# Kernel tuning notes

Measured on AMD Instinct MI355X. Metric: run time of the kernel, lower is better.

Reference implementation:

```python
import jax, jax.numpy as jnp
import numpy as np

B, S, D, H = 2, 2048, 1024, 16
DK = D // H
ROPE_BASE = 10000.0


def setup_inputs() -> dict:
    key = jax.random.key(0)
    ks = jax.random.split(key, 6)
    x = jax.random.normal(ks[0], (B, S, D), dtype=jnp.float32)
    # causal mask, broadcastable to [B,H,S,S]; masked_fill where mask==0
    mask = jnp.tril(jnp.ones((S, S), dtype=bool))[None, None]
    position_ids = jnp.tile(jnp.arange(S, dtype=jnp.int32)[None, :], (B, 1))
    sc = 1.0 / np.sqrt(D)
    Wq = jax.random.normal(ks[1], (D, D), dtype=jnp.float32) * sc
    Wk = jax.random.normal(ks[2], (D, D), dtype=jnp.float32) * sc
    Wv = jax.random.normal(ks[3], (D, D), dtype=jnp.float32) * sc
    Wo = jax.random.normal(ks[4], (D, D), dtype=jnp.float32) * sc
    bo = jnp.zeros((D,), dtype=jnp.float32)
    return {"x": x, "mask": mask, "position_ids": position_ids,
            "Wq": Wq, "Wk": Wk, "Wv": Wv, "Wo": Wo, "bo": bo}


def _rotate_half(t):
    t1, t2 = t[..., : t.shape[-1] // 2], t[..., t.shape[-1] // 2:]
    return jnp.concatenate((-t2, t1), axis=-1)


def reference(x, mask, position_ids, Wq, Wk, Wv, Wo, bo):
    b, s, d = x.shape
    h, dk = H, DK
    scale = 1.0 / np.sqrt(dk)

    def proj(W):  # torch Linear: x @ W.T -> [b,h,s,dk]
        return (x @ W.T).reshape(b, s, h, dk).transpose(0, 2, 1, 3)

    Q, K, V = proj(Wq), proj(Wk), proj(Wv)

    # rotary tables (computed in fp32, matching RotaryEmbedding)
    inv_freq = 1.0 / (ROPE_BASE ** (jnp.arange(0, dk, 2, dtype=jnp.float32) / dk))
    t = jnp.arange(s, dtype=jnp.float32)
    freqs = jnp.outer(t, inv_freq)            # [s, dk/2]
    emb = jnp.concatenate((freqs, freqs), -1) # [s, dk]
    cos = jnp.cos(emb)[position_ids][:, None]  # [b,1,s,dk]
    sin = jnp.sin(emb)[position_ids][:, None]
    Q = Q * cos + _rotate_half(Q) * sin
    K = K * cos + _rotate_half(K) * sin

    scores = jnp.einsum('bhqd,bhkd->bhqk', Q, K) * scale
    scores = jnp.where(mask, scores, jnp.float32(-1e9))
    attn = jax.nn.softmax(scores, axis=-1)  # dropout is identity in eval
    out = jnp.einsum('bhqk,bhkd->bhqd', attn, V)
    out = out.transpose(0, 2, 1, 3).reshape(b, s, d)
    return out @ Wo.T + bo
```

## Files before the change

kernel.cpp:

```cpp
#include <hip/hip_runtime.h>
#include <hip/hip_bf16.h>
#include <cstdint>

#define BB 2
#define SS 2048
#define DD 1024
#define HH 16
#define DK 64
#define MROWS (BB*SS)
#define NQKV  (3*DD)

typedef __bf16 bf16x8 __attribute__((ext_vector_type(8)));
typedef float  f32x4  __attribute__((ext_vector_type(4)));
typedef float  f32x16 __attribute__((ext_vector_type(16)));
typedef unsigned u32x2 __attribute__((ext_vector_type(2)));

static __device__ __forceinline__ unsigned short f2bf(float f) {
    __bf16 h = (__bf16)f;
    return __builtin_bit_cast(unsigned short, h);
}
static __device__ __forceinline__ float bf2f(unsigned short u) {
    return (float)__builtin_bit_cast(__bf16, u);
}

#define GLOAD16(gsrc, ldst) \
    __builtin_amdgcn_global_load_lds((const __attribute__((address_space(1))) void*)(gsrc), \
                                     (__attribute__((address_space(3))) void*)(ldst), 16, 0, 0)

static __device__ __forceinline__ void pl32_swap(unsigned &x, unsigned &y) {
#if __has_builtin(__builtin_amdgcn_permlane32_swap)
    u32x2 r = __builtin_amdgcn_permlane32_swap(x, y, false, false);
    x = r[0]; y = r[1];
#else
    asm volatile("v_permlane32_swap_b32 %0, %1" : "+v"(x), "+v"(y));
#endif
}
static __device__ __forceinline__ float swap_half(float v, bool hi) {
    unsigned x = __builtin_bit_cast(unsigned, v), y = x;
    pl32_swap(x, y);
    return __builtin_bit_cast(float, hi ? x : y);
}
template<int BASE> static __device__ __forceinline__ bf16x8 cvt_chunk(const f32x16 &p) {
    unsigned x0, y0, x1, y1;
    asm("v_cvt_pk_bf16_f32 %0, %1, %2" : "=v"(x0) : "v"(p[BASE+0]), "v"(p[BASE+1]));
    asm("v_cvt_pk_bf16_f32 %0, %1, %2" : "=v"(y0) : "v"(p[BASE+4]), "v"(p[BASE+5]));
    asm("v_cvt_pk_bf16_f32 %0, %1, %2" : "=v"(x1) : "v"(p[BASE+2]), "v"(p[BASE+3]));
    asm("v_cvt_pk_bf16_f32 %0, %1, %2" : "=v"(y1) : "v"(p[BASE+6]), "v"(p[BASE+7]));
    pl32_swap(x0, y0);
    pl32_swap(x1, y1);
    union { unsigned u[4]; bf16x8 v; } r;
    r.u[0] = x0; r.u[1] = x1; r.u[2] = y0; r.u[3] = y1;
    return r.v;
}

__global__ void cast_all(const float* __restrict__ x,  const float* __restrict__ wq,
                         const float* __restrict__ wk, const float* __restrict__ wv,
                         const float* __restrict__ wo,
                         unsigned short* __restrict__ xb, unsigned short* __restrict__ wqkv,
                         unsigned short* __restrict__ wob)
{
    const int NX = MROWS * DD;
    const int NW = DD * DD;
    const int total = (NX + 4 * NW) / 8;
    for (int i = blockIdx.x * blockDim.x + threadIdx.x; i < total; i += gridDim.x * blockDim.x) {
        int base = i * 8;
        const float* src; unsigned short* dst; int off;
        if      (base < NX)          { src = x;  dst = xb;          off = base; }
        else if (base < NX + NW)     { src = wq; dst = wqkv;        off = base - NX; }
        else if (base < NX + 2*NW)   { src = wk; dst = wqkv + NW;   off = base - NX - NW; }
        else if (base < NX + 3*NW)   { src = wv; dst = wqkv + 2*NW; off = base - NX - 2*NW; }
        else                         { src = wo; dst = wob;         off = base - NX - 3*NW; }
        float4 a = *(const float4*)(src + off);
        float4 b = *(const float4*)(src + off + 4);
        union { unsigned short s[8]; uint4 v; } u;
        u.s[0] = f2bf(a.x); u.s[1] = f2bf(a.y); u.s[2] = f2bf(a.z); u.s[3] = f2bf(a.w);
        u.s[4] = f2bf(b.x); u.s[5] = f2bf(b.y); u.s[6] = f2bf(b.z); u.s[7] = f2bf(b.w);
        *(uint4*)(dst + off) = u.v;
    }
}

__global__ void rope_table(float* __restrict__ tabc, float* __restrict__ tabs)
{
    int i = blockIdx.x * blockDim.x + threadIdx.x;
    int s = i >> 5, d = i & 31;
    float inv = exp2f(-(float)d * (13.287712379549449f / 32.f));
    float ang = (float)s * inv;
    tabc[i] = cosf(ang);
    tabs[i] = sinf(ang);
}

template<int OUTF32>
__global__ __launch_bounds__(256) void gemm_bt(
    const unsigned short* __restrict__ A, const unsigned short* __restrict__ Bm,
    void* __restrict__ Cout, const float* __restrict__ bias,
    int M, int N, int K)
{
    __shared__ __align__(16) unsigned short sA[128 * 64];
    __shared__ __align__(16) unsigned short sB[128 * 64];
    const int tid = threadIdx.x;
    const int w = tid >> 6, l = tid & 63;
    const int wm = w >> 1, wn = w & 1;
    const int lr = l & 15, lg = l >> 4;
    const int mBase = blockIdx.y * 128, nBase = blockIdx.x * 128;
    const int srow = tid >> 3;
    const int skof = (tid & 7) * 8;

    f32x4 acc[4][4] = {};

    for (int kt = 0; kt < K; kt += 64) {
        __syncthreads();
        #pragma unroll
        for (int i = 0; i < 4; ++i) {
            const unsigned short* srcA = A + (size_t)(mBase + i*32 + srow) * K + kt + skof;
            GLOAD16(srcA, &sA[i*2048 + w*512]);
            const unsigned short* srcB = Bm + (size_t)(nBase + i*32 + srow) * K + kt + skof;
            GLOAD16(srcB, &sB[i*2048 + w*512]);
        }
        __syncthreads();
        #pragma unroll
        for (int kk = 0; kk < 2; ++kk) {
            bf16x8 af[4], bfv[4];
            #pragma unroll
            for (int mi = 0; mi < 4; ++mi)
                af[mi] = *(const bf16x8*)&sA[(wm*64 + mi*16 + lr)*64 + kk*32 + lg*8];
            #pragma unroll
            for (int ni = 0; ni < 4; ++ni)
                bfv[ni] = *(const bf16x8*)&sB[(wn*64 + ni*16 + lr)*64 + kk*32 + lg*8];
            #pragma unroll
            for (int mi = 0; mi < 4; ++mi)
                #pragma unroll
                for (int ni = 0; ni < 4; ++ni)
                    acc[mi][ni] = __builtin_amdgcn_mfma_f32_16x16x32_bf16(af[mi], bfv[ni], acc[mi][ni], 0, 0, 0);
        }
    }
    #pragma unroll
    for (int mi = 0; mi < 4; ++mi) {
        #pragma unroll
        for (int j = 0; j < 4; ++j) {
            int row = mBase + wm*64 + mi*16 + lg*4 + j;
            #pragma unroll
            for (int ni = 0; ni < 4; ++ni) {
                int col = nBase + wn*64 + ni*16 + lr;
                float v = acc[mi][ni][j];
                if (OUTF32) ((float*)Cout)[(size_t)row * N + col] = v + bias[col];
                else        ((unsigned short*)Cout)[(size_t)row * N + col] = f2bf(v);
            }
        }
    }
}

__global__ void rope_qk(const unsigned short* __restrict__ qkv,
                        const int* __restrict__ pids,
                        const float* __restrict__ tabc, const float* __restrict__ tabs,
                        unsigned short* __restrict__ Qb, unsigned short* __restrict__ Kb)
{
    int i = blockIdx.x * blockDim.x + threadIdx.x;
    int cb = i & 3;
    int h  = (i >> 2) & 15;
    int isK = (i >> 6) & 1;
    int r  = i >> 7;
    int pos = pids[r];
    int dbase = cb * 8;

    const unsigned short* src = qkv + (size_t)r * NQKV + isK * DD + h * 64 + dbase;
    union { unsigned short u[8]; uint4 v; } a, bq, o1, o2;
    a.v  = *(const uint4*)src;
    bq.v = *(const uint4*)(src + 32);
    float cs[8], sn[8];
    *(float4*)&cs[0] = *(const float4*)(tabc + pos*32 + dbase);
    *(float4*)&cs[4] = *(const float4*)(tabc + pos*32 + dbase + 4);
    *(float4*)&sn[0] = *(const float4*)(tabs + pos*32 + dbase);
    *(float4*)&sn[4] = *(const float4*)(tabs + pos*32 + dbase + 4);
    float scale = isK ? 1.0f : 0.1803368801111244f;
    #pragma unroll
    for (int j = 0; j < 8; ++j) {
        float v1 = bf2f(a.u[j]), v2 = bf2f(bq.u[j]);
        o1.u[j] = f2bf((v1*cs[j] - v2*sn[j]) * scale);
        o2.u[j] = f2bf((v2*cs[j] + v1*sn[j]) * scale);
    }
    unsigned short* dst = (isK ? Kb : Qb) + (size_t)r * DD + h * 64 + dbase;
    *(uint4*)dst        = o1.v;
    *(uint4*)(dst + 32) = o2.v;
}

__global__ __launch_bounds__(256) void v_transpose(
    const unsigned short* __restrict__ qkv, unsigned short* __restrict__ Vt)
{
    __shared__ __align__(16) unsigned short sT[64 * 64];
    const int bh = blockIdx.y;
    const int st = blockIdx.x;
    const int b = bh >> 4, h = bh & 15;
    const int tid = threadIdx.x;
    #pragma unroll
    for (int i = 0; i < 2; ++i) {
        int c = tid + i*256;
        int s = c >> 3, cb = c & 7;
        const unsigned short* src = qkv + (size_t)(b*SS + st*64 + s) * NQKV + 2*DD + h*64 + cb*8;
        uint4 v = *(const uint4*)src;
        *(uint4*)&sT[s*64 + ((cb ^ (s >> 3)) * 8)] = v;
    }
    __syncthreads();
    #pragma unroll
    for (int i = 0; i < 2; ++i) {
        int c = tid + i*256;
        int d = c >> 3, sb = c & 7;
        union { unsigned short u[8]; uint4 v; } o;
        #pragma unroll
        for (int e = 0; e < 8; ++e) {
            int s = sb*8 + e;
            o.u[e] = sT[s*64 + (((d >> 3) ^ (s >> 3)) * 8) + (d & 7)];
        }
        *(uint4*)(Vt + (size_t)(bh*64 + d) * SS + st*64 + sb*8) = o.v;
    }
}

__global__ __launch_bounds__(128, 2) void attn_fwd(
    const unsigned short* __restrict__ Qb,
    const unsigned short* __restrict__ Kb,
    const unsigned short* __restrict__ Vt,
    unsigned short* __restrict__ Ob)
{
    __shared__ __align__(16) unsigned short sK[2][64 * 64];
    __shared__ __align__(16) unsigned short sV[2][64 * 64];
    const int tid = threadIdx.x;
    const int w = tid >> 6, l = tid & 63;
    const int lq = l & 31;
    const int hi5 = l >> 5;
    const bool hb = hi5 != 0;

    const int xcd = blockIdx.x & 7;
    const int c   = blockIdx.x >> 3;
    const int g   = c >> 5;
    const int s_  = c & 31;
    const int qt  = (g & 1) ? (31 - s_) : s_;
    const int bh  = xcd * 4 + g;
    const int b = bh >> 4, h = bh & 15;

    const int srow2 = tid >> 3;
    const int skof  = (tid & 7) * 8;
    const int sksw  = skof ^ ((srow2 & 7) * 8);
    const int sw    = (lq & 7) * 8;
    const float THR = 12.0f;

    const unsigned kR = (unsigned)((b*SS + srow2) * DD + h*64 + sksw);
    const unsigned vR = (unsigned)((bh*64 + srow2) * SS + sksw);

    bf16x8 qf[4];
    {
        const unsigned short* qp = Qb + (size_t)(b*SS + qt*64 + w*32 + lq) * DD + h*64 + hi5*8;
        #pragma unroll
        for (int dkc = 0; dkc < 4; ++dkc)
            qf[dkc] = *(const bf16x8*)(qp + dkc*16);
    }
    const int q_lane = qt*64 + w*32 + lq;

    f32x16 o0 = {}, o1 = {};
    float mrow = -3.0e38f, lsum = 0.f;
    int cur = 0;

    #pragma unroll
    for (int i = 0; i < 4; ++i) {
        GLOAD16(Kb + kR + (unsigned)(i << 14), &sK[0][i*1024 + w*512]);
        GLOAD16(Vt + vR + (unsigned)(i << 15), &sV[0][i*1024 + w*512]);
    }

    for (int kt = 0; kt <= qt; ++kt) {
        __syncthreads();
        if (kt < qt) {
            unsigned ko = (unsigned)(kt + 1) << 16;
            unsigned vo = (unsigned)(kt + 1) << 6;
            #pragma unroll
            for (int i = 0; i < 4; ++i) {
                GLOAD16(Kb + kR + ko + (unsigned)(i << 14), &sK[cur^1][i*1024 + w*512]);
                GLOAD16(Vt + vR + vo + (unsigned)(i << 15), &sV[cur^1][i*1024 + w*512]);
            }
        }

        f32x16 p0 = {}, p1 = {};
        __builtin_amdgcn_s_setprio(1);
        #pragma unroll
        for (int dkc = 0; dkc < 4; ++dkc) {
            bf16x8 k0 = *(const bf16x8*)&sK[cur][lq*64 + ((dkc*16 + hi5*8) ^ sw)];
            p0 = __builtin_amdgcn_mfma_f32_32x32x16_bf16(k0, qf[dkc], p0, 0, 0, 0);
        }
        #pragma unroll
        for (int dkc = 0; dkc < 4; ++dkc) {
            bf16x8 k1 = *(const bf16x8*)&sK[cur][(32 + lq)*64 + ((dkc*16 + hi5*8) ^ sw)];
            p1 = __builtin_amdgcn_mfma_f32_32x32x16_bf16(k1, qf[dkc], p1, 0, 0, 0);
        }
        __builtin_amdgcn_s_setprio(0);

        if (kt == qt) {
            const int kb0 = kt*64 + 4*hi5;
            #pragma unroll
            for (int r = 0; r < 16; ++r) {
                const int cr = (r & 3) + 8*(r >> 2);
                if (kb0 + cr > q_lane)      p0[r] = -1e30f;
                if (kb0 + 32 + cr > q_lane) p1[r] = -1e30f;
            }
        }

        float tt[16];
        #pragma unroll
        for (int r = 0; r < 16; ++r) tt[r] = fmaxf(p0[r], p1[r]);
        #pragma unroll
        for (int s2 = 8; s2 >= 1; s2 >>= 1)
            #pragma unroll
            for (int r = 0; r < 8; ++r)
                if (r < s2) tt[r] = fmaxf(tt[r], tt[r + s2]);
        float tmx = fmaxf(tt[0], swap_half(tt[0], hb));

        float growth = tmx - mrow;
        if (!__all(growth <= THR)) {
            float mnew = fmaxf(mrow, tmx);
            float alpha = exp2f(mrow - mnew);
            lsum *= alpha;
            mrow = mnew;
            #pragma unroll
            for (int r = 0; r < 16; ++r) { o0[r] *= alpha; o1[r] *= alpha; }
        }

        #pragma unroll
        for (int r = 0; r < 16; ++r) {
            p0[r] = exp2f(p0[r] - mrow);
            p1[r] = exp2f(p1[r] - mrow);
        }
        float st[16];
        #pragma unroll
        for (int r = 0; r < 16; ++r) st[r] = p0[r] + p1[r];
        #pragma unroll
        for (int s2 = 8; s2 >= 1; s2 >>= 1)
            #pragma unroll
            for (int r = 0; r < 8; ++r)
                if (r < s2) st[r] += st[r + s2];
        lsum += st[0];

        __builtin_amdgcn_s_setprio(1);
        {
            bf16x8 pa, vf;
            pa = cvt_chunk<0>(p0);
            vf = *(const bf16x8*)&sV[cur][lq*64 + ((0*16 + hi5*8) ^ sw)];
            o0 = __builtin_amdgcn_mfma_f32_32x32x16_bf16(vf, pa, o0, 0, 0, 0);
            vf = *(const bf16x8*)&sV[cur][(32 + lq)*64 + ((0*16 + hi5*8) ^ sw)];
            o1 = __builtin_amdgcn_mfma_f32_32x32x16_bf16(vf, pa, o1, 0, 0, 0);
            pa = cvt_chunk<8>(p0);
            vf = *(const bf16x8*)&sV[cur][lq*64 + ((1*16 + hi5*8) ^ sw)];
            o0 = __builtin_amdgcn_mfma_f32_32x32x16_bf16(vf, pa, o0, 0, 0, 0);
            vf = *(const bf16x8*)&sV[cur][(32 + lq)*64 + ((1*16 + hi5*8) ^ sw)];
            o1 = __builtin_amdgcn_mfma_f32_32x32x16_bf16(vf, pa, o1, 0, 0, 0);
            pa = cvt_chunk<0>(p1);
            vf = *(const bf16x8*)&sV[cur][lq*64 + ((2*16 + hi5*8) ^ sw)];
            o0 = __builtin_amdgcn_mfma_f32_32x32x16_bf16(vf, pa, o0, 0, 0, 0);
            vf = *(const bf16x8*)&sV[cur][(32 + lq)*64 + ((2*16 + hi5*8) ^ sw)];
            o1 = __builtin_amdgcn_mfma_f32_32x32x16_bf16(vf, pa, o1, 0, 0, 0);
            pa = cvt_chunk<8>(p1);
            vf = *(const bf16x8*)&sV[cur][lq*64 + ((3*16 + hi5*8) ^ sw)];
            o0 = __builtin_amdgcn_mfma_f32_32x32x16_bf16(vf, pa, o0, 0, 0, 0);
            vf = *(const bf16x8*)&sV[cur][(32 + lq)*64 + ((3*16 + hi5*8) ^ sw)];
            o1 = __builtin_amdgcn_mfma_f32_32x32x16_bf16(vf, pa, o1, 0, 0, 0);
        }
        __builtin_amdgcn_s_setprio(0);
        cur ^= 1;
    }

    __syncthreads();
    float ls = lsum + swap_half(lsum, hb);
    float inv = 1.f / ls;
    unsigned short* sO = &sK[0][0] + w * 2048;

    #pragma unroll
    for (int g2 = 0; g2 < 4; ++g2) {
        unsigned ua, ub; uint2 t2;
        float v0 = o0[g2*4+0]*inv, v1 = o0[g2*4+1]*inv, v2 = o0[g2*4+2]*inv, v3 = o0[g2*4+3]*inv;
        asm("v_cvt_pk_bf16_f32 %0, %1, %2" : "=v"(ua) : "v"(v0), "v"(v1));
        asm("v_cvt_pk_bf16_f32 %0, %1, %2" : "=v"(ub) : "v"(v2), "v"(v3));
        t2.x = ua; t2.y = ub;
        *(uint2*)&sO[lq*64 + g2*8 + hi5*4] = t2;
        float w0 = o1[g2*4+0]*inv, w1 = o1[g2*4+1]*inv, w2 = o1[g2*4+2]*inv, w3 = o1[g2*4+3]*inv;
        asm("v_cvt_pk_bf16_f32 %0, %1, %2" : "=v"(ua) : "v"(w0), "v"(w1));
        asm("v_cvt_pk_bf16_f32 %0, %1, %2" : "=v"(ub) : "v"(w2), "v"(w3));
        t2.x = ua; t2.y = ub;
        *(uint2*)&sO[lq*64 + 32 + g2*8 + hi5*4] = t2;
    }
    asm volatile("s_waitcnt lgkmcnt(0)" ::: "memory");
    __builtin_amdgcn_sched_barrier(0);

    const int row = l >> 1, cb2 = (l & 1) * 32;
    const unsigned short* sOr = sO + row*64 + cb2;
    unsigned short* gp = Ob + (size_t)(b*SS + qt*64 + w*32 + row) * DD + h*64 + cb2;
    #pragma unroll
    for (int c2 = 0; c2 < 4; ++c2)
        *(uint4*)(gp + c2*8) = *(const uint4*)(sOr + c2*8);
}

extern "C" void kernel_launch(void* const* d_in, const int* in_sizes, int n_in,
                              void* d_out, int out_size, void* d_ws, size_t ws_size,
                              hipStream_t stream)
{
    const float* x  = (const float*)d_in[0];
    const int* pids = (const int*)d_in[2];
    const float* wq = (const float*)d_in[3];
    const float* wk = (const float*)d_in[4];
    const float* wv = (const float*)d_in[5];
    const float* wo = (const float*)d_in[6];
    const float* bo = (const float*)d_in[7];
    float* out = (float*)d_out;

    char* ws = (char*)d_ws;
    unsigned short* xb   = (unsigned short*)(ws);
    unsigned short* wqkv = (unsigned short*)(ws + (size_t)( 8u<<20));
    unsigned short* wob  = (unsigned short*)(ws + (size_t)(14u<<20));
    unsigned short* qkvp = (unsigned short*)(ws + (size_t)(16u<<20));
    unsigned short* Qb   = (unsigned short*)(ws + (size_t)(40u<<20));
    unsigned short* Kb   = (unsigned short*)(ws + (size_t)(48u<<20));
    unsigned short* Vt   = (unsigned short*)(ws + (size_t)(56u<<20));
    float* tabc          = (float*)(ws + (size_t)(64u<<20));
    float* tabs          = (float*)(ws + (size_t)(64u<<20) + (256u<<10));
    unsigned short* Ob   = xb;

    cast_all<<<dim3(4096), dim3(256), 0, stream>>>(x, wq, wk, wv, wo, xb, wqkv, wob);
    rope_table<<<dim3(256), dim3(256), 0, stream>>>(tabc, tabs);
    gemm_bt<0><<<dim3(NQKV/128, MROWS/128), dim3(256), 0, stream>>>(
        xb, wqkv, (void*)qkvp, (const float*)nullptr, MROWS, NQKV, DD);
    rope_qk<<<dim3(2048), dim3(256), 0, stream>>>(qkvp, pids, tabc, tabs, Qb, Kb);
    v_transpose<<<dim3(32, 32), dim3(256), 0, stream>>>(qkvp, Vt);
    attn_fwd<<<dim3(1024), dim3(128), 0, stream>>>(Qb, Kb, Vt, Ob);
    gemm_bt<1><<<dim3(DD/128, MROWS/128), dim3(256), 0, stream>>>(
        Ob, wob, (void*)out, bo, MROWS, DD, DD);
}
```

Measured before the change: 154.2 us.

## Fuse RoPE into QKV GEMM epilogue and swizzle GEMM block order

The RoPE rotation and Q scaling move into the QKV projection GEMM epilogue, using the fact that each 64-column wave tile holds one head so the d and d+32 pairs sit in the same thread's accumulators. This removes the separate rope_qk kernel and the round trip of Q and K through the intermediate qkv buffer. V is now written to its own buffer. Both GEMMs also switch to a 1D grid with an XCD-aware swizzle of block indices, meant to improve L2 locality across the chiplets. The epilogue stores are scalar 2-byte writes, so the fused kernel may write less efficiently than the old vectorized rope kernel.

```diff
diff --git a/kernel.cpp b/kernel.cpp
--- a/kernel.cpp
+++ b/kernel.cpp
@@ -89,11 +89,12 @@
     tabs[i] = sinf(ang);
 }
 
-template<int OUTF32>
-__global__ __launch_bounds__(256) void gemm_bt(
+__global__ __launch_bounds__(256) void gemm_qkv(
     const unsigned short* __restrict__ A, const unsigned short* __restrict__ Bm,
-    void* __restrict__ Cout, const float* __restrict__ bias,
-    int M, int N, int K)
+    const int* __restrict__ pids,
+    const float* __restrict__ tabc, const float* __restrict__ tabs,
+    unsigned short* __restrict__ Qb, unsigned short* __restrict__ Kb,
+    unsigned short* __restrict__ Vr)
 {
     __shared__ __align__(16) unsigned short sA[128 * 64];
     __shared__ __align__(16) unsigned short sB[128 * 64];
@@ -101,7 +102,96 @@
     const int w = tid >> 6, l = tid & 63;
     const int wm = w >> 1, wn = w & 1;
     const int lr = l & 15, lg = l >> 4;
-    const int mBase = blockIdx.y * 128, nBase = blockIdx.x * 128;
+    const int swz = (blockIdx.x & 7) * 96 + (blockIdx.x >> 3);
+    const int bx = swz % 24, by = swz / 24;
+    const int mBase = by * 128, nBase = bx * 128;
+    const int srow = tid >> 3;
+    const int skof = (tid & 7) * 8;
+
+    f32x4 acc[4][4] = {};
+
+    for (int kt = 0; kt < DD; kt += 64) {
+        __syncthreads();
+        #pragma unroll
+        for (int i = 0; i < 4; ++i) {
+            const unsigned short* srcA = A + (size_t)(mBase + i*32 + srow) * DD + kt + skof;
+            GLOAD16(srcA, &sA[i*2048 + w*512]);
+            const unsigned short* srcB = Bm + (size_t)(nBase + i*32 + srow) * DD + kt + skof;
+            GLOAD16(srcB, &sB[i*2048 + w*512]);
+        }
+        __syncthreads();
+        #pragma unroll
+        for (int kk = 0; kk < 2; ++kk) {
+            bf16x8 af[4], bfv[4];
+            #pragma unroll
+            for (int mi = 0; mi < 4; ++mi)
+                af[mi] = *(const bf16x8*)&sA[(wm*64 + mi*16 + lr)*64 + kk*32 + lg*8];
+            #pragma unroll
+            for (int ni = 0; ni < 4; ++ni)
+                bfv[ni] = *(const bf16x8*)&sB[(wn*64 + ni*16 + lr)*64 + kk*32 + lg*8];
+            #pragma unroll
+            for (int mi = 0; mi < 4; ++mi)
+                #pragma unroll
+                for (int ni = 0; ni < 4; ++ni)
+                    acc[mi][ni] = __builtin_amdgcn_mfma_f32_16x16x32_bf16(af[mi], bfv[ni], acc[mi][ni], 0, 0, 0);
+        }
+    }
+
+    if (bx < 16) {
+        const bool isQ = bx < 8;
+        unsigned short* dst = isQ ? Qb : Kb;
+        const float qsc = isQ ? 0.1803368801111244f : 1.0f;
+        const int colbase = (bx & 7)*128 + wn*64;
+        #pragma unroll
+        for (int mi = 0; mi < 4; ++mi) {
+            #pragma unroll
+            for (int j = 0; j < 4; ++j) {
+                int row = mBase + wm*64 + mi*16 + lg*4 + j;
+                int pos = pids[row];
+                #pragma unroll
+                for (int ni = 0; ni < 2; ++ni) {
+                    int d = ni*16 + lr;
+                    float cc = tabc[pos*32 + d];
+                    float sn = tabs[pos*32 + d];
+                    float a  = acc[mi][ni][j];
+                    float bb = acc[mi][ni+2][j];
+                    dst[(size_t)row * DD + colbase + d]      = f2bf((a*cc - bb*sn) * qsc);
+                    dst[(size_t)row * DD + colbase + d + 32] = f2bf((bb*cc + a*sn) * qsc);
+                }
+            }
+        }
+    } else {
+        const int colbase = (bx - 16)*128 + wn*64;
+        #pragma unroll
+        for (int mi = 0; mi < 4; ++mi) {
+            #pragma unroll
+            for (int j = 0; j < 4; ++j) {
+                int row = mBase + wm*64 + mi*16 + lg*4 + j;
+                #pragma unroll
+                for (int ni = 0; ni < 4; ++ni)
+                    Vr[(size_t)row * DD + colbase + ni*16 + lr] = f2bf(acc[mi][ni][j]);
+            }
+        }
+    }
+}
+
+__global__ __launch_bounds__(256) void gemm_bt(
+    const unsigned short* __restrict__ A, const unsigned short* __restrict__ Bm,
+    float* __restrict__ Cout, const float* __restrict__ bias,
+    int M, int N, int K)
+{
+    __shared__ __align__(16) unsigned short sA[128 * 64];
+    __shared__ __align__(16) unsigned short sB[128 * 64];
+    const int tid = threadIdx.x;
+    const int w = tid >> 6, l = tid & 63;
+    const int wm = w >> 1, wn = w & 1;
+    const int lr = l & 15, lg = l >> 4;
+    const int nwg = gridDim.x;
+    const int cpx = nwg >> 3;
+    const int swz = (blockIdx.x & 7) * cpx + (blockIdx.x >> 3);
+    const int nbx = N >> 7;
+    const int bx = swz % nbx, by = swz / nbx;
+    const int mBase = by * 128, nBase = bx * 128;
     const int srow = tid >> 3;
     const int skof = (tid & 7) * 8;
 
@@ -141,50 +231,14 @@
             #pragma unroll
             for (int ni = 0; ni < 4; ++ni) {
                 int col = nBase + wn*64 + ni*16 + lr;
-                float v = acc[mi][ni][j];
-                if (OUTF32) ((float*)Cout)[(size_t)row * N + col] = v + bias[col];
-                else        ((unsigned short*)Cout)[(size_t)row * N + col] = f2bf(v);
+                Cout[(size_t)row * N + col] = acc[mi][ni][j] + bias[col];
             }
         }
     }
 }
 
-__global__ void rope_qk(const unsigned short* __restrict__ qkv,
-                        const int* __restrict__ pids,
-                        const float* __restrict__ tabc, const float* __restrict__ tabs,
-                        unsigned short* __restrict__ Qb, unsigned short* __restrict__ Kb)
-{
-    int i = blockIdx.x * blockDim.x + threadIdx.x;
-    int cb = i & 3;
-    int h  = (i >> 2) & 15;
-    int isK = (i >> 6) & 1;
-    int r  = i >> 7;
-    int pos = pids[r];
-    int dbase = cb * 8;
-
-    const unsigned short* src = qkv + (size_t)r * NQKV + isK * DD + h * 64 + dbase;
-    union { unsigned short u[8]; uint4 v; } a, bq, o1, o2;
-    a.v  = *(const uint4*)src;
-    bq.v = *(const uint4*)(src + 32);
-    float cs[8], sn[8];
-    *(float4*)&cs[0] = *(const float4*)(tabc + pos*32 + dbase);
-    *(float4*)&cs[4] = *(const float4*)(tabc + pos*32 + dbase + 4);
-    *(float4*)&sn[0] = *(const float4*)(tabs + pos*32 + dbase);
-    *(float4*)&sn[4] = *(const float4*)(tabs + pos*32 + dbase + 4);
-    float scale = isK ? 1.0f : 0.1803368801111244f;
-    #pragma unroll
-    for (int j = 0; j < 8; ++j) {
-        float v1 = bf2f(a.u[j]), v2 = bf2f(bq.u[j]);
-        o1.u[j] = f2bf((v1*cs[j] - v2*sn[j]) * scale);
-        o2.u[j] = f2bf((v2*cs[j] + v1*sn[j]) * scale);
-    }
-    unsigned short* dst = (isK ? Kb : Qb) + (size_t)r * DD + h * 64 + dbase;
-    *(uint4*)dst        = o1.v;
-    *(uint4*)(dst + 32) = o2.v;
-}
-
 __global__ __launch_bounds__(256) void v_transpose(
-    const unsigned short* __restrict__ qkv, unsigned short* __restrict__ Vt)
+    const unsigned short* __restrict__ Vr, unsigned short* __restrict__ Vt)
 {
     __shared__ __align__(16) unsigned short sT[64 * 64];
     const int bh = blockIdx.y;
@@ -195,7 +249,7 @@
     for (int i = 0; i < 2; ++i) {
         int c = tid + i*256;
         int s = c >> 3, cb = c & 7;
-        const unsigned short* src = qkv + (size_t)(b*SS + st*64 + s) * NQKV + 2*DD + h*64 + cb*8;
+        const unsigned short* src = Vr + (size_t)(b*SS + st*64 + s) * DD + h*64 + cb*8;
         uint4 v = *(const uint4*)src;
         *(uint4*)&sT[s*64 + ((cb ^ (s >> 3)) * 8)] = v;
     }
@@ -410,7 +464,7 @@
     unsigned short* xb   = (unsigned short*)(ws);
     unsigned short* wqkv = (unsigned short*)(ws + (size_t)( 8u<<20));
     unsigned short* wob  = (unsigned short*)(ws + (size_t)(14u<<20));
-    unsigned short* qkvp = (unsigned short*)(ws + (size_t)(16u<<20));
+    unsigned short* Vr   = (unsigned short*)(ws + (size_t)(16u<<20));
     unsigned short* Qb   = (unsigned short*)(ws + (size_t)(40u<<20));
     unsigned short* Kb   = (unsigned short*)(ws + (size_t)(48u<<20));
     unsigned short* Vt   = (unsigned short*)(ws + (size_t)(56u<<20));
@@ -420,11 +474,10 @@
 
     cast_all<<<dim3(4096), dim3(256), 0, stream>>>(x, wq, wk, wv, wo, xb, wqkv, wob);
     rope_table<<<dim3(256), dim3(256), 0, stream>>>(tabc, tabs);
-    gemm_bt<0><<<dim3(NQKV/128, MROWS/128), dim3(256), 0, stream>>>(
-        xb, wqkv, (void*)qkvp, (const float*)nullptr, MROWS, NQKV, DD);
-    rope_qk<<<dim3(2048), dim3(256), 0, stream>>>(qkvp, pids, tabc, tabs, Qb, Kb);
-    v_transpose<<<dim3(32, 32), dim3(256), 0, stream>>>(qkvp, Vt);
+    gemm_qkv<<<dim3(768), dim3(256), 0, stream>>>(
+        xb, wqkv, pids, tabc, tabs, Qb, Kb, Vr);
+    v_transpose<<<dim3(32, 32), dim3(256), 0, stream>>>(Vr, Vt);
     attn_fwd<<<dim3(1024), dim3(128), 0, stream>>>(Qb, Kb, Vt, Ob);
-    gemm_bt<1><<<dim3(DD/128, MROWS/128), dim3(256), 0, stream>>>(
-        Ob, wob, (void*)out, bo, MROWS, DD, DD);
-}
+    gemm_bt<<<dim3(256), dim3(256), 0, stream>>>(
+        Ob, wob, out, bo, MROWS, DD, DD);
+}
```

Measured after the change: 151.5 us. No clear change (-1.7%).
